# Performance work log

Hardware: AMD Instinct MI355X
Metric: run time of the kernel (lower is better)

The kernel has to match this reference:

```python
import jax, jax.numpy as jnp
import numpy as np

WINDOW_SIZE = 11
SIGMA = 1.5
C1 = 0.01 ** 2
C2 = 0.03 ** 2


def _gaussian_window(channel, dtype):
    # 1D gaussian, normalized, then outer product -> 2D window [ws, ws]
    center = WINDOW_SIZE // 2
    x = jnp.arange(WINDOW_SIZE, dtype=jnp.float32) - center
    g = jnp.exp(-(x ** 2) / (2.0 * SIGMA ** 2))
    g = g / g.sum()
    w2d = jnp.outer(g, g)  # [ws, ws]
    # depthwise kernel: [C_out=channel, C_in/groups=1, ws, ws]
    return jnp.broadcast_to(w2d, (channel, 1, WINDOW_SIZE, WINDOW_SIZE)).astype(dtype)


def _depthwise_blur(x, window):
    pad = WINDOW_SIZE // 2
    return jax.lax.conv_general_dilated(
        x, window,
        window_strides=(1, 1),
        padding=[(pad, pad), (pad, pad)],
        feature_group_count=x.shape[1],
        dimension_numbers=('NCHW', 'OIHW', 'NCHW'))


def setup_inputs() -> dict:
    key = jax.random.key(0)
    k1, k2 = jax.random.split(key)
    img1 = jax.random.uniform(k1, (16, 3, 512, 512), dtype=jnp.float32)
    img2 = jax.random.uniform(k2, (16, 3, 512, 512), dtype=jnp.float32)
    return {"img1": img1, "img2": img2}


def reference(img1, img2):
    channel = img1.shape[1]
    window = _gaussian_window(channel, img1.dtype)

    mu1 = _depthwise_blur(img1, window)
    mu2 = _depthwise_blur(img2, window)
    mu1_sq = mu1 * mu1
    mu2_sq = mu2 * mu2
    mu1_mu2 = mu1 * mu2

    sigma1_sq = _depthwise_blur(img1 * img1, window) - mu1_sq
    sigma2_sq = _depthwise_blur(img2 * img2, window) - mu2_sq
    sigma12 = _depthwise_blur(img1 * img2, window) - mu1_mu2

    ssim_map = ((2.0 * mu1_mu2 + C1) * (2.0 * sigma12 + C2)) / (
        (mu1_sq + mu2_sq + C1) * (sigma1_sq + sigma2_sq + C2))
    return ssim_map.mean()  # size_average=True
```

## Files before the change

kernel.cpp:

```cpp
#include <hip/hip_runtime.h>


typedef _Float16 f16;
typedef __attribute__((ext_vector_type(4))) _Float16 f16x4;
typedef __attribute__((ext_vector_type(8))) _Float16 f16x8;
typedef __attribute__((ext_vector_type(4))) float f32x4;

#define IMGW 512
#define IMGH 512
#define NPL 48
#define NBLOCKS (NPL * 8 * 8)
#define NPIX 12582912.0
#define REDT 1024

#define SR 84
#define NC 80
#define IMGOFF (NC * SR)

#define INV_T 0.99967202f

__device__ const float G_dev[11] = {0.00102838f, 0.00759876f, 0.03600077f,
                                    0.10936069f, 0.21300554f, 0.26601172f,
                                    0.21300554f, 0.10936069f, 0.03600077f,
                                    0.00759876f, 0.00102838f};

template<bool EDGE>
__device__ __forceinline__ void stage(const float* __restrict__ p1,
                                      const float* __restrict__ p2,
                                      int R0, int AC0, int tid, f16* sT) {
    #pragma unroll
    for (int it = 0; it < 13; ++it) {
        const int idx = tid + it * 256;
        if (it == 12 && idx >= 3200) break;
        const int img  = (idx >= 1600) ? 1 : 0;
        const int rem  = idx - img * 1600;
        const int g    = rem / NC;
        const int lcol = rem - g * NC;
        const float* __restrict__ base = img ? p2 : p1;
        const int gc = AC0 + lcol;
        const int gr = R0 + 4 * g;
        float v[4];
        if (EDGE) {
            const bool cok = ((unsigned)gc < (unsigned)IMGW);
            const int cc = cok ? gc : 0;
            #pragma unroll
            for (int e = 0; e < 4; ++e) {
                const int r  = gr + e;
                const bool ok = cok && ((unsigned)r < (unsigned)IMGH);
                const int rc = (r < 0) ? 0 : (r > IMGH - 1 ? IMGH - 1 : r);
                const float x = base[(size_t)rc * IMGW + cc];
                v[e] = ok ? x : 0.0f;
            }
        } else {
            #pragma unroll
            for (int e = 0; e < 4; ++e)
                v[e] = base[(size_t)(gr + e) * IMGW + gc];
        }
        const f16x4 h = {(f16)v[0], (f16)v[1], (f16)v[2], (f16)v[3]};
        *(f16x4*)&sT[(size_t)img * IMGOFF + (size_t)lcol * SR + 4 * g] = h;
    }
}

__global__ __launch_bounds__(256, 4) void ssim_main(const float* __restrict__ img1,
                                                    const float* __restrict__ img2,
                                                    float* __restrict__ partial) {
    __shared__ f16 sT[2 * IMGOFF];
    __shared__ float wsum[4];

    const int tid  = threadIdx.x;
    const int lane = tid & 63;
    const int wv   = tid >> 6;
    const int l15  = lane & 15;
    const int lg   = lane >> 4;

    const int bid   = blockIdx.x;
    const int plane = bid >> 6;
    const int rem   = bid & 63;
    const int by    = rem >> 3;
    const int bx    = rem & 7;
    const int r0b   = by * 64;
    const int c0    = bx * 64;
    const int R0    = r0b - 5;
    const int AC0   = c0 - 8;

    const float* __restrict__ p1 = img1 + (size_t)plane * (IMGH * IMGW);
    const float* __restrict__ p2 = img2 + (size_t)plane * (IMGH * IMGW);

    if (by >= 1 && by <= 6 && bx >= 1 && bx <= 6)
        stage<false>(p1, p2, R0, AC0, tid, sT);
    else
        stage<true >(p1, p2, R0, AC0, tid, sT);
    __syncthreads();

    f16x8 bband;
    #pragma unroll
    for (int j = 0; j < 8; ++j) {
        const int kj = (j < 4) ? (4 * lg + j) : (16 + 4 * lg + (j - 4));
        const int t  = kj - l15;
        const float w = (t >= 0 && t < 11) ? G_dev[t] : 0.0f;
        bband[j] = (f16)w;
    }

    const f32x4 zero4 = {0.0f, 0.0f, 0.0f, 0.0f};

    f16x4 hv[5][5];
    #pragma unroll
    for (int t = 0; t < 5; ++t) {
        int col = 3 + 16 * t + l15;
        if (t == 4) col = (col > NC - 1) ? NC - 1 : col;
        const int ro = 16 * wv + 4 * lg;
        const f16* __restrict__ cb1 = sT + (size_t)col * SR;
        const f16* __restrict__ cb2 = sT + IMGOFF + (size_t)col * SR;
        const f16x4 xlo = *(const f16x4*)&cb1[ro];
        const f16x4 xhi = *(const f16x4*)&cb1[ro + 16];
        const f16x4 ylo = *(const f16x4*)&cb2[ro];
        const f16x4 yhi = *(const f16x4*)&cb2[ro + 16];
        const f16x8 fx = __builtin_shufflevector(xlo, xhi, 0, 1, 2, 3, 4, 5, 6, 7);
        const f16x8 fy = __builtin_shufflevector(ylo, yhi, 0, 1, 2, 3, 4, 5, 6, 7);
        const f16x8 fxx = fx * fx;
        const f16x8 fyy = fy * fy;
        const f16x8 fxy = fx * fy;

        const f32x4 dx  = __builtin_amdgcn_mfma_f32_16x16x32_f16(fx,  bband, zero4, 0, 0, 0);
        const f32x4 dy  = __builtin_amdgcn_mfma_f32_16x16x32_f16(fy,  bband, zero4, 0, 0, 0);
        const f32x4 dxx = __builtin_amdgcn_mfma_f32_16x16x32_f16(fxx, bband, zero4, 0, 0, 0);
        const f32x4 dyy = __builtin_amdgcn_mfma_f32_16x16x32_f16(fyy, bband, zero4, 0, 0, 0);
        const f32x4 dxy = __builtin_amdgcn_mfma_f32_16x16x32_f16(fxy, bband, zero4, 0, 0, 0);

        hv[t][0] = (f16x4){(f16)dx[0],  (f16)dx[1],  (f16)dx[2],  (f16)dx[3]};
        hv[t][1] = (f16x4){(f16)dy[0],  (f16)dy[1],  (f16)dy[2],  (f16)dy[3]};
        hv[t][2] = (f16x4){(f16)dxx[0], (f16)dxx[1], (f16)dxx[2], (f16)dxx[3]};
        hv[t][3] = (f16x4){(f16)dyy[0], (f16)dyy[1], (f16)dyy[2], (f16)dyy[3]};
        hv[t][4] = (f16x4){(f16)dxy[0], (f16)dxy[1], (f16)dxy[2], (f16)dxy[3]};
    }

    float acc = 0.0f;
    const float C1 = 1.0e-4f;
    const float C2 = 9.0e-4f;
    #pragma unroll
    for (int m = 0; m < 4; ++m) {
        f32x4 h[5];
        #pragma unroll
        for (int q = 0; q < 5; ++q) {
            const f16x8 a = __builtin_shufflevector(hv[m][q], hv[m + 1][q],
                                                    0, 1, 2, 3, 4, 5, 6, 7);
            h[q] = __builtin_amdgcn_mfma_f32_16x16x32_f16(a, bband, zero4, 0, 0, 0);
            h[q] *= INV_T;
        }
        #pragma unroll
        for (int r = 0; r < 4; ++r) {
            const float mu1 = h[0][r], mu2 = h[1][r];
            const float exx = h[2][r], eyy = h[3][r], exy = h[4][r];
            const float mu1s = mu1 * mu1;
            const float mu2s = mu2 * mu2;
            const float mu12 = mu1 * mu2;
            const float s1  = exx - mu1s;
            const float s2  = eyy - mu2s;
            const float s12 = exy - mu12;
            const float num = fmaf(2.0f, mu12, C1) * fmaf(2.0f, s12, C2);
            const float den = (mu1s + mu2s + C1) * (s1 + s2 + C2);
            float rd = __builtin_amdgcn_rcpf(den);
            rd = rd * fmaf(-den, rd, 2.0f);
            acc = fmaf(num, rd, acc);
        }
    }

    #pragma unroll
    for (int off = 32; off > 0; off >>= 1)
        acc += __shfl_down(acc, off, 64);
    if (lane == 0) wsum[wv] = acc;
    __syncthreads();
    if (tid == 0)
        partial[bid] = (wsum[0] + wsum[1]) + (wsum[2] + wsum[3]);
}

__global__ __launch_bounds__(REDT) void ssim_reduce(const float* __restrict__ partial,
                                                    float* __restrict__ out) {
    const int tid = threadIdx.x;
    double s = 0.0;
    for (int i = tid; i < NBLOCKS; i += REDT)
        s += (double)partial[i];
    #pragma unroll
    for (int off = 32; off > 0; off >>= 1)
        s += __shfl_down(s, off, 64);
    __shared__ double wsd[REDT / 64];
    if ((tid & 63) == 0) wsd[tid >> 6] = s;
    __syncthreads();
    if (tid == 0) {
        double t = 0.0;
        #pragma unroll
        for (int i = 0; i < REDT / 64; ++i) t += wsd[i];
        out[0] = (float)(t / NPIX);
    }
}

extern "C" void kernel_launch(void* const* d_in, const int* in_sizes, int n_in,
                              void* d_out, int out_size, void* d_ws, size_t ws_size,
                              hipStream_t stream) {
    const float* img1 = (const float*)d_in[0];
    const float* img2 = (const float*)d_in[1];
    float* partial = (float*)d_ws;
    float* out = (float*)d_out;
    ssim_main<<<NBLOCKS, 256, 0, stream>>>(img1, img2, partial);
    ssim_reduce<<<1, REDT, 0, stream>>>(partial, out);
}
```

Measured before the change: 50.48 us.

## Make blocks persistent over four row tiles with register-prefetched loads

Each block now processes four vertically stacked 64x64 tiles instead of one, which cuts the grid by a factor of four. Global loads for the next tile are issued into registers before the current tile's MFMA compute, then written to shared memory after it, so memory latency overlaps with compute. This adds register pressure (launch bounds lowered from 4 to 3 blocks per CU) and leaves fewer blocks to hide latency and balance load across CUs.

```diff
diff --git a/kernel.cpp b/kernel.cpp
--- a/kernel.cpp
+++ b/kernel.cpp
@@ -9,7 +9,8 @@
 #define IMGW 512
 #define IMGH 512
 #define NPL 48
-#define NBLOCKS (NPL * 8 * 8)
+#define PT 4
+#define NBLOCKS (NPL * 8 * 2)
 #define NPIX 12582912.0
 #define REDT 1024
 
@@ -25,13 +26,13 @@
                                     0.00759876f, 0.00102838f};
 
 template<bool EDGE>
-__device__ __forceinline__ void stage(const float* __restrict__ p1,
+__device__ __forceinline__ void issue(const float* __restrict__ p1,
                                       const float* __restrict__ p2,
-                                      int R0, int AC0, int tid, f16* sT) {
+                                      int R0, int AC0, int tid, float v[13][4]) {
     #pragma unroll
     for (int it = 0; it < 13; ++it) {
-        const int idx = tid + it * 256;
-        if (it == 12 && idx >= 3200) break;
+        if (it == 12 && tid >= 128) break;
+        const int idx  = tid + it * 256;
         const int img  = (idx >= 1600) ? 1 : 0;
         const int rem  = idx - img * 1600;
         const int g    = rem / NC;
@@ -39,7 +40,6 @@
         const float* __restrict__ base = img ? p2 : p1;
         const int gc = AC0 + lcol;
         const int gr = R0 + 4 * g;
-        float v[4];
         if (EDGE) {
             const bool cok = ((unsigned)gc < (unsigned)IMGW);
             const int cc = cok ? gc : 0;
@@ -49,60 +49,33 @@
                 const bool ok = cok && ((unsigned)r < (unsigned)IMGH);
                 const int rc = (r < 0) ? 0 : (r > IMGH - 1 ? IMGH - 1 : r);
                 const float x = base[(size_t)rc * IMGW + cc];
-                v[e] = ok ? x : 0.0f;
+                v[it][e] = ok ? x : 0.0f;
             }
         } else {
             #pragma unroll
             for (int e = 0; e < 4; ++e)
-                v[e] = base[(size_t)(gr + e) * IMGW + gc];
-        }
-        const f16x4 h = {(f16)v[0], (f16)v[1], (f16)v[2], (f16)v[3]};
+                v[it][e] = base[(size_t)(gr + e) * IMGW + gc];
+        }
+    }
+}
+
+__device__ __forceinline__ void commit(const float v[13][4], int tid, f16* sT) {
+    #pragma unroll
+    for (int it = 0; it < 13; ++it) {
+        if (it == 12 && tid >= 128) break;
+        const int idx  = tid + it * 256;
+        const int img  = (idx >= 1600) ? 1 : 0;
+        const int rem  = idx - img * 1600;
+        const int g    = rem / NC;
+        const int lcol = rem - g * NC;
+        const f16x4 h = {(f16)v[it][0], (f16)v[it][1], (f16)v[it][2], (f16)v[it][3]};
         *(f16x4*)&sT[(size_t)img * IMGOFF + (size_t)lcol * SR + 4 * g] = h;
     }
 }
 
-__global__ __launch_bounds__(256, 4) void ssim_main(const float* __restrict__ img1,
-                                                    const float* __restrict__ img2,
-                                                    float* __restrict__ partial) {
-    __shared__ f16 sT[2 * IMGOFF];
-    __shared__ float wsum[4];
-
-    const int tid  = threadIdx.x;
-    const int lane = tid & 63;
-    const int wv   = tid >> 6;
-    const int l15  = lane & 15;
-    const int lg   = lane >> 4;
-
-    const int bid   = blockIdx.x;
-    const int plane = bid >> 6;
-    const int rem   = bid & 63;
-    const int by    = rem >> 3;
-    const int bx    = rem & 7;
-    const int r0b   = by * 64;
-    const int c0    = bx * 64;
-    const int R0    = r0b - 5;
-    const int AC0   = c0 - 8;
-
-    const float* __restrict__ p1 = img1 + (size_t)plane * (IMGH * IMGW);
-    const float* __restrict__ p2 = img2 + (size_t)plane * (IMGH * IMGW);
-
-    if (by >= 1 && by <= 6 && bx >= 1 && bx <= 6)
-        stage<false>(p1, p2, R0, AC0, tid, sT);
-    else
-        stage<true >(p1, p2, R0, AC0, tid, sT);
-    __syncthreads();
-
-    f16x8 bband;
-    #pragma unroll
-    for (int j = 0; j < 8; ++j) {
-        const int kj = (j < 4) ? (4 * lg + j) : (16 + 4 * lg + (j - 4));
-        const int t  = kj - l15;
-        const float w = (t >= 0 && t < 11) ? G_dev[t] : 0.0f;
-        bband[j] = (f16)w;
-    }
-
+__device__ __forceinline__ float compute_tile(const f16* sT, int wv, int l15,
+                                              int lg, f16x8 bband) {
     const f32x4 zero4 = {0.0f, 0.0f, 0.0f, 0.0f};
-
     f16x4 hv[5][5];
     #pragma unroll
     for (int t = 0; t < 5; ++t) {
@@ -164,6 +137,64 @@
             acc = fmaf(num, rd, acc);
         }
     }
+    return acc;
+}
+
+__global__ __launch_bounds__(256, 3) void ssim_main(const float* __restrict__ img1,
+                                                    const float* __restrict__ img2,
+                                                    float* __restrict__ partial) {
+    __shared__ f16 sT[2 * IMGOFF];
+    __shared__ float wsum[4];
+
+    const int tid  = threadIdx.x;
+    const int lane = tid & 63;
+    const int wv   = tid >> 6;
+    const int l15  = lane & 15;
+    const int lg   = lane >> 4;
+
+    const int bid   = blockIdx.x;
+    const int plane = bid >> 4;
+    const int rem   = bid & 15;
+    const int half  = rem >> 3;
+    const int bx    = rem & 7;
+    const int c0    = bx * 64;
+    const int AC0   = c0 - 8;
+    const bool colEdge = (bx == 0) || (bx == 7);
+
+    const float* __restrict__ p1 = img1 + (size_t)plane * (IMGH * IMGW);
+    const float* __restrict__ p2 = img2 + (size_t)plane * (IMGH * IMGW);
+
+    f16x8 bband;
+    #pragma unroll
+    for (int j = 0; j < 8; ++j) {
+        const int kj = (j < 4) ? (4 * lg + j) : (16 + 4 * lg + (j - 4));
+        const int t  = kj - l15;
+        const float w = (t >= 0 && t < 11) ? G_dev[t] : 0.0f;
+        bband[j] = (f16)w;
+    }
+
+    float v[13][4];
+    float acc = 0.0f;
+
+    {
+        const int R0 = half * 256 - 5;
+        if (colEdge || half == 0) issue<true >(p1, p2, R0, AC0, tid, v);
+        else                      issue<false>(p1, p2, R0, AC0, tid, v);
+    }
+
+    #pragma unroll
+    for (int t = 0; t < PT; ++t) {
+        commit(v, tid, sT);
+        __syncthreads();
+        if (t < PT - 1) {
+            const int R0n = half * 256 + (t + 1) * 64 - 5;
+            const bool en = colEdge || (half == 1 && t + 1 == PT - 1);
+            if (en) issue<true >(p1, p2, R0n, AC0, tid, v);
+            else    issue<false>(p1, p2, R0n, AC0, tid, v);
+        }
+        acc += compute_tile(sT, wv, l15, lg, bband);
+        __syncthreads();
+    }
 
     #pragma unroll
     for (int off = 32; off > 0; off >>= 1)
```

Result: slower. 79.93 us (+58.3%).
